# Optimization experiments

Hardware: AMD Instinct MI355X
Metric: run time of the kernel (lower is better)

## Reference

```python
import jax, jax.numpy as jnp
import numpy as np

B, T, IN = 4096, 512, 1
H, L = 50, 2


def setup_inputs() -> dict:
    key = jax.random.key(0)
    ks = jax.random.split(key, 11)
    s_in = 1.0 / np.sqrt(H)  # PyTorch LSTM init scale
    def u(k, shape):
        return jax.random.uniform(k, shape, jnp.float32, -s_in, s_in)
    return {
        "x": jax.random.normal(ks[0], (B, T, IN), jnp.float32),
        # layer 0 (gate order i, f, g, o stacked along first axis, like torch)
        "W_ih0": u(ks[1], (4 * H, IN)),
        "W_hh0": u(ks[2], (4 * H, H)),
        "b_ih0": u(ks[3], (4 * H,)),
        "b_hh0": u(ks[4], (4 * H,)),
        # layer 1
        "W_ih1": u(ks[5], (4 * H, H)),
        "W_hh1": u(ks[6], (4 * H, H)),
        "b_ih1": u(ks[7], (4 * H,)),
        "b_hh1": u(ks[8], (4 * H,)),
        # final linear projection hidden -> 1
        "fc_w": u(ks[9], (1, H)),
        "fc_b": u(ks[10], (1,)),
    }


def _lstm_layer(x_tbf, W_ih, W_hh, b_ih, b_hh):
    """x_tbf: [T, B, F] -> outputs [T, B, H]. Zero initial (h, c)."""
    # Precompute input contribution for all timesteps at once: [T, B, 4H]
    gates_x = jnp.einsum('tbf,gf->tbg', x_tbf, W_ih) + b_ih + b_hh

    def step(carry, gx):
        h, c = carry
        g = gx + h @ W_hh.T  # [B, 4H]
        i, f, gg, o = jnp.split(g, 4, axis=-1)
        i = jax.nn.sigmoid(i)
        f = jax.nn.sigmoid(f)
        gg = jnp.tanh(gg)
        o = jax.nn.sigmoid(o)
        c = f * c + i * gg
        h = o * jnp.tanh(c)
        return (h, c), h

    Bsz = x_tbf.shape[1]
    h0 = jnp.zeros((Bsz, W_hh.shape[1]), x_tbf.dtype)
    (_, _), hs = jax.lax.scan(step, (h0, h0), gates_x)
    return hs  # [T, B, H]


def reference(x, W_ih0, W_hh0, b_ih0, b_hh0, W_ih1, W_hh1, b_ih1, b_hh1, fc_w, fc_b):
    x_tbf = jnp.transpose(x, (1, 0, 2))  # [T, B, IN]
    h1 = _lstm_layer(x_tbf, W_ih0, W_hh0, b_ih0, b_hh0)   # [T, B, H]
    h2 = _lstm_layer(h1, W_ih1, W_hh1, b_ih1, b_hh1)      # [T, B, H]
    last = h2[-1]                                         # [B, H] == out[:, -1, :]
    return last @ fc_w.T + fc_b                           # [B, 1]
```

## Files before the change

### kernel.cpp

```cpp
#include <hip/hip_runtime.h>


typedef _Float16 half8 __attribute__((ext_vector_type(8)));
typedef float    f32x4 __attribute__((ext_vector_type(4)));

#define TT    512
#define HID   50
#define NB    16
#define XST   17
#define LOG2E 1.44269504f

__device__ __forceinline__ float4 make_wfrag(const float* W, int gate, int cell,
                                             int chunk, int quad, float scale) {
    half8 hv = {};
    #pragma unroll
    for (int j = 0; j < 8; ++j) {
        const int k = 32 * chunk + 8 * quad + j;
        float v = 0.0f;
        if (cell < HID && k < HID) v = W[(gate * HID + cell) * HID + k] * scale;
        hv[j] = (_Float16)v;
    }
    return __builtin_bit_cast(float4, hv);
}

__device__ __forceinline__ float cell_update(const f32x4 a, float& ct) {
    const float K  = 2.0f * LOG2E;
    const float ei = __builtin_amdgcn_exp2f(a[0]);
    const float ef = __builtin_amdgcn_exp2f(a[1]);
    const float eg = __builtin_amdgcn_exp2f(a[2]);
    const float eo = __builtin_amdgcn_exp2f(a[3]);
    const float p  = (1.0f + ei) * (1.0f + eg);
    const float q  = 1.0f + ef;
    const float t1 = __builtin_fmaf(eg, K, -K);
    const float num = __builtin_fmaf(ct, p, t1 * q);
    ct = num * __builtin_amdgcn_rcpf(p * q);
    const float ec = __builtin_amdgcn_exp2f(ct);
    return (ec - 1.0f) *
        __builtin_amdgcn_rcpf((1.0f + eo) * (ec + 1.0f));
}

#define PIN(f) asm volatile("" : "+v"(f.x), "+v"(f.y), "+v"(f.z), "+v"(f.w));
#define MFMA(af, b, c) __builtin_amdgcn_mfma_f32_16x16x32_f16(__builtin_bit_cast(half8, (af)), (b), (c), 0, 0, 0)

extern "C" __global__ __launch_bounds__(832, 4)
void lstm2_mfma_kernel(const float* __restrict__ x,
                       const float* __restrict__ W_ih0, const float* __restrict__ W_hh0,
                       const float* __restrict__ b_ih0, const float* __restrict__ b_hh0,
                       const float* __restrict__ W_ih1, const float* __restrict__ W_hh1,
                       const float* __restrict__ b_ih1, const float* __restrict__ b_hh1,
                       const float* __restrict__ fc_w, const float* __restrict__ fc_b,
                       float* __restrict__ out)
{
    __shared__ _Float16 H0[2][1024];
    __shared__ _Float16 H1[2][1024];
    __shared__ float    xs[TT * XST];
    __shared__ float    hfin[52 * NB];

    const int tid  = threadIdx.x;
    const int lane = tid & 63;
    const int wv   = tid >> 6;
    const int b0   = blockIdx.x * NB;

    for (int i = tid; i < 1024; i += 832) {
        H0[0][i] = (_Float16)0.f; H0[1][i] = (_Float16)0.f;
        H1[0][i] = (_Float16)0.f; H1[1][i] = (_Float16)0.f;
    }
    for (int i = tid; i < NB * TT; i += 832) {
        const int row = i >> 9;
        const int uu  = i & (TT - 1);
        xs[uu * XST + row] = x[(size_t)(b0 + row) * TT + uu];
    }

    const int quad = lane >> 4;
    const int col  = lane & 15;

    const int mrow  = lane & 15;
    const int gateA = mrow & 3;
    const int cellA = 4 * wv + (mrow >> 2);
    const float scA = (gateA == 2) ? 2.0f * LOG2E : -LOG2E;
    float4 A0c0 = make_wfrag(W_hh0, gateA, cellA, 0, quad, scA);
    float4 A0c1 = make_wfrag(W_hh0, gateA, cellA, 1, quad, scA);
    float4 Aic0 = make_wfrag(W_ih1, gateA, cellA, 0, quad, scA);
    float4 Aic1 = make_wfrag(W_ih1, gateA, cellA, 1, quad, scA);
    float4 Ahc0 = make_wfrag(W_hh1, gateA, cellA, 0, quad, scA);
    float4 Ahc1 = make_wfrag(W_hh1, gateA, cellA, 1, quad, scA);
    PIN(A0c0) PIN(A0c1) PIN(Aic0) PIN(Aic1) PIN(Ahc0) PIN(Ahc1)

    const int  cellD = 4 * wv + quad;
    const bool ewok  = (cellD < HID);
    f32x4 bias0, bias1, wx0;
    #pragma unroll
    for (int g = 0; g < 4; ++g) {
        const float s = (g == 2) ? 2.0f * LOG2E : -LOG2E;
        bias0[g] = ewok ? (b_ih0[g * HID + cellD] + b_hh0[g * HID + cellD]) * s : 0.f;
        bias1[g] = ewok ? (b_ih1[g * HID + cellD] + b_hh1[g * HID + cellD]) * s : 0.f;
        wx0[g]   = ewok ? W_ih0[g * HID + cellD] * s : 0.f;
    }
    const int wi = (cellD >> 5) * 512 + (((cellD & 31) >> 3) * 16 + col) * 8 + (cellD & 7);

    float ct0 = 0.f, ct1 = 0.f;
    __syncthreads();

    {
        const float xr = xs[col];
        f32x4 acc;
        #pragma unroll
        for (int g = 0; g < 4; ++g) acc[g] = __builtin_fmaf(wx0[g], xr, bias0[g]);
        const float h = cell_update(acc, ct0);
        H0[1][wi] = (_Float16)h;
        __syncthreads();
    }

    #pragma unroll 2
    for (int u = 1; u < TT; ++u) {
        const int pu = u & 1, pn = pu ^ 1;

        const half8 b0c0 = *(const half8*)(&H0[pu][lane * 8]);
        const half8 b0c1 = *(const half8*)(&H0[pu][512 + lane * 8]);
        const half8 b1c0 = *(const half8*)(&H1[pn][lane * 8]);
        const half8 b1c1 = *(const half8*)(&H1[pn][512 + lane * 8]);
        const float xr   = xs[u * XST + col];

        f32x4 t;
        #pragma unroll
        for (int g = 0; g < 4; ++g) t[g] = __builtin_fmaf(wx0[g], xr, bias0[g]);
        f32x4 acc0 = MFMA(A0c0, b0c0, t);
        acc0 = MFMA(A0c1, b0c1, acc0);

        f32x4 acc1 = MFMA(Aic0, b0c0, bias1);
        acc1 = MFMA(Aic1, b0c1, acc1);
        acc1 = MFMA(Ahc0, b1c0, acc1);
        acc1 = MFMA(Ahc1, b1c1, acc1);

        const float h0n = cell_update(acc0, ct0);
        H0[pn][wi] = (_Float16)h0n;
        const float h1n = cell_update(acc1, ct1);
        H1[pu][wi] = (_Float16)h1n;
        __syncthreads();
    }

    {
        const half8 b0c0 = *(const half8*)(&H0[0][lane * 8]);
        const half8 b0c1 = *(const half8*)(&H0[0][512 + lane * 8]);
        const half8 b1c0 = *(const half8*)(&H1[1][lane * 8]);
        const half8 b1c1 = *(const half8*)(&H1[1][512 + lane * 8]);
        f32x4 acc1 = MFMA(Aic0, b0c0, bias1);
        acc1 = MFMA(Aic1, b0c1, acc1);
        acc1 = MFMA(Ahc0, b1c0, acc1);
        acc1 = MFMA(Ahc1, b1c1, acc1);
        const float h1n = cell_update(acc1, ct1);
        hfin[cellD * NB + col] = h1n;
        __syncthreads();
    }

    if (tid < NB) {
        float s = fc_b[0];
        for (int k = 0; k < HID; ++k)
            s += fc_w[k] * hfin[k * NB + tid];
        out[b0 + tid] = s;
    }
}

extern "C" void kernel_launch(void* const* d_in, const int* in_sizes, int n_in,
                              void* d_out, int out_size, void* d_ws, size_t ws_size,
                              hipStream_t stream) {
    (void)in_sizes; (void)n_in; (void)d_ws; (void)ws_size; (void)out_size;
    const float* x     = (const float*)d_in[0];
    const float* W_ih0 = (const float*)d_in[1];
    const float* W_hh0 = (const float*)d_in[2];
    const float* b_ih0 = (const float*)d_in[3];
    const float* b_hh0 = (const float*)d_in[4];
    const float* W_ih1 = (const float*)d_in[5];
    const float* W_hh1 = (const float*)d_in[6];
    const float* b_ih1 = (const float*)d_in[7];
    const float* b_hh1 = (const float*)d_in[8];
    const float* fc_w  = (const float*)d_in[9];
    const float* fc_b  = (const float*)d_in[10];

    dim3 grid(4096 / NB);
    dim3 block(832);
    lstm2_mfma_kernel<<<grid, block, 0, stream>>>(
        x, W_ih0, W_hh0, b_ih0, b_hh0,
        W_ih1, W_hh1, b_ih1, b_hh1,
        fc_w, fc_b, (float*)d_out);
}
```

Baseline: 386.9 us.

## Give each wave two cell tiles, shrinking blocks from 13 to 7 waves

Each wavefront now handles two groups of four hidden cells, so a block needs 7 waves (448 threads) instead of 13. Every per-tile item (weight fragments, biases, cell state, write index) becomes a small array of two, and the per-step MFMAs and cell updates are interleaved across both tiles. The intent is to cut the cost of the per-timestep block barrier and to give each wave independent MFMA chains that hide latency. The trade-off is double the register pressure per wave and a lower declared occupancy (launch bounds of 2 instead of 4), which could reduce how much the CU overlaps work across blocks.

```diff
diff --git a/kernel.cpp b/kernel.cpp
--- a/kernel.cpp
+++ b/kernel.cpp
@@ -8,6 +8,9 @@
 #define HID   50
 #define NB    16
 #define XST   17
+#define NW    7
+#define NT    2
+#define NTHR  (NW * 64)
 #define LOG2E 1.44269504f
 
 __device__ __forceinline__ float4 make_wfrag(const float* W, int gate, int cell,
@@ -42,7 +45,7 @@
 #define PIN(f) asm volatile("" : "+v"(f.x), "+v"(f.y), "+v"(f.z), "+v"(f.w));
 #define MFMA(af, b, c) __builtin_amdgcn_mfma_f32_16x16x32_f16(__builtin_bit_cast(half8, (af)), (b), (c), 0, 0, 0)
 
-extern "C" __global__ __launch_bounds__(832, 4)
+extern "C" __global__ __launch_bounds__(NTHR, 2)
 void lstm2_mfma_kernel(const float* __restrict__ x,
                        const float* __restrict__ W_ih0, const float* __restrict__ W_hh0,
                        const float* __restrict__ b_ih0, const float* __restrict__ b_hh0,
@@ -54,18 +57,18 @@
     __shared__ _Float16 H0[2][1024];
     __shared__ _Float16 H1[2][1024];
     __shared__ float    xs[TT * XST];
-    __shared__ float    hfin[52 * NB];
+    __shared__ float    hfin[56 * NB];
 
     const int tid  = threadIdx.x;
     const int lane = tid & 63;
     const int wv   = tid >> 6;
     const int b0   = blockIdx.x * NB;
 
-    for (int i = tid; i < 1024; i += 832) {
+    for (int i = tid; i < 1024; i += NTHR) {
         H0[0][i] = (_Float16)0.f; H0[1][i] = (_Float16)0.f;
         H1[0][i] = (_Float16)0.f; H1[1][i] = (_Float16)0.f;
     }
-    for (int i = tid; i < NB * TT; i += 832) {
+    for (int i = tid; i < NB * TT; i += NTHR) {
         const int row = i >> 9;
         const int uu  = i & (TT - 1);
         xs[uu * XST + row] = x[(size_t)(b0 + row) * TT + uu];
@@ -73,41 +76,55 @@
 
     const int quad = lane >> 4;
     const int col  = lane & 15;
-
-    const int mrow  = lane & 15;
+    const int mrow = lane & 15;
     const int gateA = mrow & 3;
-    const int cellA = 4 * wv + (mrow >> 2);
     const float scA = (gateA == 2) ? 2.0f * LOG2E : -LOG2E;
-    float4 A0c0 = make_wfrag(W_hh0, gateA, cellA, 0, quad, scA);
-    float4 A0c1 = make_wfrag(W_hh0, gateA, cellA, 1, quad, scA);
-    float4 Aic0 = make_wfrag(W_ih1, gateA, cellA, 0, quad, scA);
-    float4 Aic1 = make_wfrag(W_ih1, gateA, cellA, 1, quad, scA);
-    float4 Ahc0 = make_wfrag(W_hh1, gateA, cellA, 0, quad, scA);
-    float4 Ahc1 = make_wfrag(W_hh1, gateA, cellA, 1, quad, scA);
-    PIN(A0c0) PIN(A0c1) PIN(Aic0) PIN(Aic1) PIN(Ahc0) PIN(Ahc1)
-
-    const int  cellD = 4 * wv + quad;
-    const bool ewok  = (cellD < HID);
-    f32x4 bias0, bias1, wx0;
+
+    float4 A0c0[NT], A0c1[NT], Aic0[NT], Aic1[NT], Ahc0[NT], Ahc1[NT];
+    f32x4  bias0[NT], bias1[NT], wx0[NT];
+    int    wiT[NT], cdT[NT];
     #pragma unroll
-    for (int g = 0; g < 4; ++g) {
-        const float s = (g == 2) ? 2.0f * LOG2E : -LOG2E;
-        bias0[g] = ewok ? (b_ih0[g * HID + cellD] + b_hh0[g * HID + cellD]) * s : 0.f;
-        bias1[g] = ewok ? (b_ih1[g * HID + cellD] + b_hh1[g * HID + cellD]) * s : 0.f;
-        wx0[g]   = ewok ? W_ih0[g * HID + cellD] * s : 0.f;
-    }
-    const int wi = (cellD >> 5) * 512 + (((cellD & 31) >> 3) * 16 + col) * 8 + (cellD & 7);
-
-    float ct0 = 0.f, ct1 = 0.f;
+    for (int t = 0; t < NT; ++t) {
+        const int g = NT * wv + t;
+        const int cellA = 4 * g + (mrow >> 2);
+        A0c0[t] = make_wfrag(W_hh0, gateA, cellA, 0, quad, scA);
+        A0c1[t] = make_wfrag(W_hh0, gateA, cellA, 1, quad, scA);
+        Aic0[t] = make_wfrag(W_ih1, gateA, cellA, 0, quad, scA);
+        Aic1[t] = make_wfrag(W_ih1, gateA, cellA, 1, quad, scA);
+        Ahc0[t] = make_wfrag(W_hh1, gateA, cellA, 0, quad, scA);
+        Ahc1[t] = make_wfrag(W_hh1, gateA, cellA, 1, quad, scA);
+
+        const int  cellD = 4 * g + quad;
+        const bool ewok  = (cellD < HID);
+        cdT[t] = cellD;
+        #pragma unroll
+        for (int gg = 0; gg < 4; ++gg) {
+            const float s = (gg == 2) ? 2.0f * LOG2E : -LOG2E;
+            bias0[t][gg] = ewok ? (b_ih0[gg * HID + cellD] + b_hh0[gg * HID + cellD]) * s : 0.f;
+            bias1[t][gg] = ewok ? (b_ih1[gg * HID + cellD] + b_hh1[gg * HID + cellD]) * s : 0.f;
+            wx0[t][gg]   = ewok ? W_ih0[gg * HID + cellD] * s : 0.f;
+        }
+        wiT[t] = (cellD >> 5) * 512 + (((cellD & 31) >> 3) * 16 + col) * 8 + (cellD & 7);
+    }
+    #pragma unroll
+    for (int t = 0; t < NT; ++t) {
+        PIN(A0c0[t]) PIN(A0c1[t]) PIN(Aic0[t]) PIN(Aic1[t]) PIN(Ahc0[t]) PIN(Ahc1[t])
+    }
+
+    float ct0[NT] = {0.f, 0.f}, ct1[NT] = {0.f, 0.f};
     __syncthreads();
 
     {
         const float xr = xs[col];
-        f32x4 acc;
-        #pragma unroll
-        for (int g = 0; g < 4; ++g) acc[g] = __builtin_fmaf(wx0[g], xr, bias0[g]);
-        const float h = cell_update(acc, ct0);
-        H0[1][wi] = (_Float16)h;
+        #pragma unroll
+        for (int t = 0; t < NT; ++t) {
+            f32x4 acc;
+            #pragma unroll
+            for (int gg = 0; gg < 4; ++gg)
+                acc[gg] = __builtin_fmaf(wx0[t][gg], xr, bias0[t][gg]);
+            const float h = cell_update(acc, ct0[t]);
+            H0[1][wiT[t]] = (_Float16)h;
+        }
         __syncthreads();
     }
 
@@ -121,21 +138,27 @@
         const half8 b1c1 = *(const half8*)(&H1[pn][512 + lane * 8]);
         const float xr   = xs[u * XST + col];
 
-        f32x4 t;
-        #pragma unroll
-        for (int g = 0; g < 4; ++g) t[g] = __builtin_fmaf(wx0[g], xr, bias0[g]);
-        f32x4 acc0 = MFMA(A0c0, b0c0, t);
-        acc0 = MFMA(A0c1, b0c1, acc0);
-
-        f32x4 acc1 = MFMA(Aic0, b0c0, bias1);
-        acc1 = MFMA(Aic1, b0c1, acc1);
-        acc1 = MFMA(Ahc0, b1c0, acc1);
-        acc1 = MFMA(Ahc1, b1c1, acc1);
-
-        const float h0n = cell_update(acc0, ct0);
-        H0[pn][wi] = (_Float16)h0n;
-        const float h1n = cell_update(acc1, ct1);
-        H1[pu][wi] = (_Float16)h1n;
+        f32x4 acc0[NT], acc1[NT];
+        #pragma unroll
+        for (int t = 0; t < NT; ++t) {
+            f32x4 tv;
+            #pragma unroll
+            for (int gg = 0; gg < 4; ++gg)
+                tv[gg] = __builtin_fmaf(wx0[t][gg], xr, bias0[t][gg]);
+            acc0[t] = MFMA(A0c0[t], b0c0, tv);
+            acc0[t] = MFMA(A0c1[t], b0c1, acc0[t]);
+            acc1[t] = MFMA(Aic0[t], b0c0, bias1[t]);
+            acc1[t] = MFMA(Aic1[t], b0c1, acc1[t]);
+            acc1[t] = MFMA(Ahc0[t], b1c0, acc1[t]);
+            acc1[t] = MFMA(Ahc1[t], b1c1, acc1[t]);
+        }
+        #pragma unroll
+        for (int t = 0; t < NT; ++t) {
+            const float h0n = cell_update(acc0[t], ct0[t]);
+            H0[pn][wiT[t]] = (_Float16)h0n;
+            const float h1n = cell_update(acc1[t], ct1[t]);
+            H1[pu][wiT[t]] = (_Float16)h1n;
+        }
         __syncthreads();
     }
 
@@ -144,12 +167,15 @@
         const half8 b0c1 = *(const half8*)(&H0[0][512 + lane * 8]);
         const half8 b1c0 = *(const half8*)(&H1[1][lane * 8]);
         const half8 b1c1 = *(const half8*)(&H1[1][512 + lane * 8]);
-        f32x4 acc1 = MFMA(Aic0, b0c0, bias1);
-        acc1 = MFMA(Aic1, b0c1, acc1);
-        acc1 = MFMA(Ahc0, b1c0, acc1);
-        acc1 = MFMA(Ahc1, b1c1, acc1);
-        const float h1n = cell_update(acc1, ct1);
-        hfin[cellD * NB + col] = h1n;
+        #pragma unroll
+        for (int t = 0; t < NT; ++t) {
+            f32x4 acc1 = MFMA(Aic0[t], b0c0, bias1[t]);
+            acc1 = MFMA(Aic1[t], b0c1, acc1);
+            acc1 = MFMA(Ahc0[t], b1c0, acc1);
+            acc1 = MFMA(Ahc1[t], b1c1, acc1);
+            const float h1n = cell_update(acc1, ct1[t]);
+            hfin[cdT[t] * NB + col] = h1n;
+        }
         __syncthreads();
     }
 
@@ -178,7 +204,7 @@
     const float* fc_b  = (const float*)d_in[10];
 
     dim3 grid(4096 / NB);
-    dim3 block(832);
+    dim3 block(NTHR);
     lstm2_mfma_kernel<<<grid, block, 0, stream>>>(
         x, W_ih0, W_hh0, b_ih0, b_hh0,
         W_ih1, W_hh1, b_ih1, b_hh1,
```

New measurement: 415.1 us. 7.3% more time.

## Split waves into two groups to overlap deferred cell updates with MFMAs

Applied to the files above, without the earlier changes.

Waves are split into two groups by the hidden-cell range they own, matching the two K-chunks of the recurrent MFMAs. Group A (cells 0-31) applies its cell update right away. Group B (cells 32-49) stores its gate accumulators and applies the update in the next step, while the chunk-0 MFMAs, which depend only on group A's outputs, are already running. This shortens the serial dependency between time steps but adds a second block-wide barrier per step, plus extra prologue and epilogue code.

```diff
diff --git a/kernel.cpp b/kernel.cpp
--- a/kernel.cpp
+++ b/kernel.cpp
@@ -73,11 +73,11 @@
 
     const int quad = lane >> 4;
     const int col  = lane & 15;
-
-    const int mrow  = lane & 15;
+    const int mrow = lane & 15;
     const int gateA = mrow & 3;
     const int cellA = 4 * wv + (mrow >> 2);
     const float scA = (gateA == 2) ? 2.0f * LOG2E : -LOG2E;
+
     float4 A0c0 = make_wfrag(W_hh0, gateA, cellA, 0, quad, scA);
     float4 A0c1 = make_wfrag(W_hh0, gateA, cellA, 1, quad, scA);
     float4 Aic0 = make_wfrag(W_ih1, gateA, cellA, 0, quad, scA);
@@ -88,6 +88,7 @@
 
     const int  cellD = 4 * wv + quad;
     const bool ewok  = (cellD < HID);
+    const bool grpA  = (wv < 8);
     f32x4 bias0, bias1, wx0;
     #pragma unroll
     for (int g = 0; g < 4; ++g) {
@@ -99,59 +100,108 @@
     const int wi = (cellD >> 5) * 512 + (((cellD & 31) >> 3) * 16 + col) * 8 + (cellD & 7);
 
     float ct0 = 0.f, ct1 = 0.f;
+    f32x4 sv0 = {0.f, 0.f, 0.f, 0.f};
+    f32x4 sv1 = {0.f, 0.f, 0.f, 0.f};
     __syncthreads();
 
     {
         const float xr = xs[col];
-        f32x4 acc;
+        f32x4 a;
         #pragma unroll
-        for (int g = 0; g < 4; ++g) acc[g] = __builtin_fmaf(wx0[g], xr, bias0[g]);
-        const float h = cell_update(acc, ct0);
-        H0[1][wi] = (_Float16)h;
-        __syncthreads();
-    }
-
-    #pragma unroll 2
-    for (int u = 1; u < TT; ++u) {
-        const int pu = u & 1, pn = pu ^ 1;
-
-        const half8 b0c0 = *(const half8*)(&H0[pu][lane * 8]);
-        const half8 b0c1 = *(const half8*)(&H0[pu][512 + lane * 8]);
-        const half8 b1c0 = *(const half8*)(&H1[pn][lane * 8]);
-        const half8 b1c1 = *(const half8*)(&H1[pn][512 + lane * 8]);
-        const float xr   = xs[u * XST + col];
-
+        for (int g = 0; g < 4; ++g) a[g] = __builtin_fmaf(wx0[g], xr, bias0[g]);
+        if (grpA) {
+            const float h = cell_update(a, ct0);
+            H0[1][wi] = (_Float16)h;
+        } else {
+            sv0 = a;
+        }
+    }
+    __syncthreads();
+
+    {
+        const half8 b0c0 = *(const half8*)(&H0[1][lane * 8]);
+        const half8 b1c0 = *(const half8*)(&H1[0][lane * 8]);
+        const float xr   = xs[XST + col];
         f32x4 t;
         #pragma unroll
         for (int g = 0; g < 4; ++g) t[g] = __builtin_fmaf(wx0[g], xr, bias0[g]);
         f32x4 acc0 = MFMA(A0c0, b0c0, t);
+        f32x4 acc1 = MFMA(Aic0, b0c0, bias1);
+        acc1 = MFMA(Ahc0, b1c0, acc1);
+        if (!grpA) {
+            const float h = cell_update(sv0, ct0);
+            H0[1][wi] = (_Float16)h;
+        }
+        __syncthreads();
+        const half8 b0c1 = *(const half8*)(&H0[1][512 + lane * 8]);
+        const half8 b1c1 = *(const half8*)(&H1[0][512 + lane * 8]);
         acc0 = MFMA(A0c1, b0c1, acc0);
-
+        acc1 = MFMA(Aic1, b0c1, acc1);
+        acc1 = MFMA(Ahc1, b1c1, acc1);
+        if (grpA) {
+            const float h0n = cell_update(acc0, ct0);
+            H0[0][wi] = (_Float16)h0n;
+            const float h1n = cell_update(acc1, ct1);
+            H1[1][wi] = (_Float16)h1n;
+        } else { sv0 = acc0; sv1 = acc1; }
+        __syncthreads();
+    }
+
+    #pragma unroll 2
+    for (int u = 2; u < TT; ++u) {
+        const int pu = u & 1, pn = pu ^ 1;
+
+        const half8 b0c0 = *(const half8*)(&H0[pu][lane * 8]);
+        const half8 b1c0 = *(const half8*)(&H1[pn][lane * 8]);
+        const float xr   = xs[u * XST + col];
+        f32x4 t;
+        #pragma unroll
+        for (int g = 0; g < 4; ++g) t[g] = __builtin_fmaf(wx0[g], xr, bias0[g]);
+        f32x4 acc0 = MFMA(A0c0, b0c0, t);
         f32x4 acc1 = MFMA(Aic0, b0c0, bias1);
+        acc1 = MFMA(Ahc0, b1c0, acc1);
+        if (!grpA) {
+            const float h0n = cell_update(sv0, ct0);
+            H0[pu][wi] = (_Float16)h0n;
+            const float h1n = cell_update(sv1, ct1);
+            H1[pn][wi] = (_Float16)h1n;
+        }
+        __syncthreads();
+
+        const half8 b0c1 = *(const half8*)(&H0[pu][512 + lane * 8]);
+        const half8 b1c1 = *(const half8*)(&H1[pn][512 + lane * 8]);
+        acc0 = MFMA(A0c1, b0c1, acc0);
         acc1 = MFMA(Aic1, b0c1, acc1);
-        acc1 = MFMA(Ahc0, b1c0, acc1);
         acc1 = MFMA(Ahc1, b1c1, acc1);
-
-        const float h0n = cell_update(acc0, ct0);
-        H0[pn][wi] = (_Float16)h0n;
-        const float h1n = cell_update(acc1, ct1);
-        H1[pu][wi] = (_Float16)h1n;
+        if (grpA) {
+            const float h0n = cell_update(acc0, ct0);
+            H0[pn][wi] = (_Float16)h0n;
+            const float h1n = cell_update(acc1, ct1);
+            H1[pu][wi] = (_Float16)h1n;
+        } else { sv0 = acc0; sv1 = acc1; }
         __syncthreads();
     }
 
     {
         const half8 b0c0 = *(const half8*)(&H0[0][lane * 8]);
+        const half8 b1c0 = *(const half8*)(&H1[1][lane * 8]);
+        f32x4 acc1 = MFMA(Aic0, b0c0, bias1);
+        acc1 = MFMA(Ahc0, b1c0, acc1);
+        if (!grpA) {
+            const float h0n = cell_update(sv0, ct0);
+            H0[0][wi] = (_Float16)h0n;
+            const float h1n = cell_update(sv1, ct1);
+            H1[1][wi] = (_Float16)h1n;
+        }
+        __syncthreads();
         const half8 b0c1 = *(const half8*)(&H0[0][512 + lane * 8]);
-        const half8 b1c0 = *(const half8*)(&H1[1][lane * 8]);
         const half8 b1c1 = *(const half8*)(&H1[1][512 + lane * 8]);
-        f32x4 acc1 = MFMA(Aic0, b0c0, bias1);
         acc1 = MFMA(Aic1, b0c1, acc1);
-        acc1 = MFMA(Ahc0, b1c0, acc1);
         acc1 = MFMA(Ahc1, b1c1, acc1);
         const float h1n = cell_update(acc1, ct1);
         hfin[cellD * NB + col] = h1n;
-        __syncthreads();
-    }
+    }
+    __syncthreads();
 
     if (tid < NB) {
         float s = fc_b[0];
```

Result: slower. 435.3 us (+12.5%).
